# Kernel tuning notes

Measured on AMD Instinct MI355X. Metric: run time of the kernel, lower is better.

Reference implementation:

```python
import jax, jax.numpy as jnp
import numpy as np

FEATURES = 1024
EXPANDED = 16
HIDDEN = FEATURES * EXPANDED  # 16384
BATCH = 4096


def setup_inputs() -> dict:
    key = jax.random.key(0)
    k_x, k_we, k_be, k_wd, k_bd = jax.random.split(key, 5)
    s_enc = 1.0 / np.sqrt(FEATURES)
    s_dec = 1.0 / np.sqrt(HIDDEN)
    return {
        "x": jax.random.normal(k_x, (BATCH, FEATURES), dtype=jnp.float32),
        "W_enc": jax.random.uniform(k_we, (HIDDEN, FEATURES), jnp.float32, -s_enc, s_enc),
        "b_enc": jax.random.uniform(k_be, (HIDDEN,), jnp.float32, -s_enc, s_enc),
        "W_dec": jax.random.uniform(k_wd, (FEATURES, HIDDEN), jnp.float32, -s_dec, s_dec),
        "b_dec": jax.random.uniform(k_bd, (FEATURES,), jnp.float32, -s_dec, s_dec),
        "activate": 64,
    }


def reference(x, W_enc, b_enc, W_dec, b_dec, activate):
    # Encoder: subtract decoder bias, dense GEMM -> pre-activations a [B, HIDDEN]
    xbar = x - b_dec
    a = jnp.einsum("bf,hf->bh", xbar, W_enc) + b_enc
    # TopK per row, relu values, scatter back into a zero tensor
    vals, idx = jax.lax.top_k(a, activate)           # [B, k]
    f = jnp.zeros_like(a)
    rows = jnp.arange(a.shape[0])[:, None]           # [B, 1]
    f = f.at[rows, idx].set(jax.nn.relu(vals))
    # Decoder: dense GEMM back to feature space (faithful to original dense decode)
    xhat = jnp.einsum("bh,fh->bf", f, W_dec) + b_dec
    return f, xhat
```

## Files before the change

kernel.cpp:

```cpp
#include <hip/hip_runtime.h>
#include <cstdint>

#define B_ 4096
#define F_ 1024
#define H_ 16384
#define TOPK 64
#define MAXC 192
#define NBINS 2048
#define BINW 0.00390625f
#define TWOE 0.020f

typedef unsigned short u16;
typedef __attribute__((ext_vector_type(8))) _Float16 f16x8;
typedef __attribute__((ext_vector_type(8))) unsigned short u16x8;
typedef __attribute__((ext_vector_type(4))) float f32x4;

__device__ __forceinline__ u16 f2bf(float f) {
  union { float f; uint32_t u; } v; v.f = f;
  uint32_t u = v.u;
  uint32_t r = u + 0x7FFFu + ((u >> 16) & 1u);
  return (u16)(r >> 16);
}
__device__ __forceinline__ float bf2f(u16 h) {
  union { uint32_t u; float f; } v; v.u = ((uint32_t)h) << 16; return v.f;
}
__device__ __forceinline__ u16 f2h(float f) {
  union { _Float16 h; u16 u; } v; v.h = (_Float16)f; return v.u;
}
__device__ __forceinline__ float h2f(u16 h) {
  union { _Float16 h; u16 u; } v; v.u = h; return (float)v.h;
}

__device__ __forceinline__ void async16(const void* g, void* l) {
  __builtin_amdgcn_global_load_lds(
      reinterpret_cast<const __attribute__((address_space(1))) uint32_t*>(
          reinterpret_cast<uintptr_t>(g)),
      reinterpret_cast<__attribute__((address_space(3))) uint32_t*>(
          reinterpret_cast<uintptr_t>(l)),
      16, 0, 0);
}

__global__ __launch_bounds__(256) void k_xbar(const float* __restrict__ x,
                                              const float* __restrict__ b_dec,
                                              u16* __restrict__ xbar) {
  int i = blockIdx.x * 256 + threadIdx.x;
  int base = i * 4;
  int col = base & (F_ - 1);
  float4 xv = *(const float4*)(x + base);
  float4 bv = *(const float4*)(b_dec + col);
  ushort4 o;
  o.x = f2h(xv.x - bv.x); o.y = f2h(xv.y - bv.y);
  o.z = f2h(xv.z - bv.z); o.w = f2h(xv.w - bv.w);
  *(ushort4*)(xbar + base) = o;
}

__global__ __launch_bounds__(256) void k_cast(const float* __restrict__ src,
                                              u16* __restrict__ dst) {
  size_t base = (size_t)(blockIdx.x * 256 + threadIdx.x) * 4;
  float4 v = *(const float4*)(src + base);
  ushort4 o; o.x = f2h(v.x); o.y = f2h(v.y); o.z = f2h(v.z); o.w = f2h(v.w);
  *(ushort4*)(dst + base) = o;
}

__global__ __launch_bounds__(256) void k_transpose(const float* __restrict__ Wdec,
                                                   u16* __restrict__ WdecT) {
  __shared__ float tile[32][33];
  int hb = blockIdx.x * 32, fb = blockIdx.y * 32;
  int tx = threadIdx.x & 31, ty = threadIdx.x >> 5;
#pragma unroll
  for (int i = 0; i < 32; i += 8)
    tile[ty + i][tx] = Wdec[(size_t)(fb + ty + i) * H_ + hb + tx];
  __syncthreads();
#pragma unroll
  for (int i = 0; i < 32; i += 8)
    WdecT[(size_t)(hb + ty + i) * F_ + fb + tx] = f2bf(tile[tx][ty + i]);
}

__global__ __launch_bounds__(256) void k_gemm(const u16* __restrict__ A,
                                              const u16* __restrict__ Bm,
                                              const float* __restrict__ b_enc,
                                              u16* __restrict__ Cf16,
                                              float* __restrict__ fzero) {
  __shared__ u16 lA[128 * 32];
  __shared__ u16 lB[128 * 32];
  const int tid = threadIdx.x;
  const int lane = tid & 63, wave = tid >> 6;
  const int wm = wave >> 1, wn = wave & 1;
  const int bx = blockIdx.x, by = blockIdx.y;

  const int kcs = (tid & 3) ^ ((tid >> 3) & 3);
  const u16* gA0 = A + (size_t)(by * 128 + (tid >> 2)) * F_ + kcs * 8;
  const u16* gB0 = Bm + (size_t)(bx * 128 + (tid >> 2)) * F_ + kcs * 8;
  u16* lA0 = &lA[tid * 8];
  u16* lB0 = &lB[tid * 8];

  f32x4 acc[4][4] = {};
  const int lm = lane & 15;
  const int kcp = (((lane >> 4) ^ ((lm >> 1) & 3))) * 8;

  for (int k0 = 0; k0 < F_; k0 += 32) {
    async16(gA0 + k0, lA0);
    async16(gA0 + 64 * F_ + k0, lA0 + 2048);
    async16(gB0 + k0, lB0);
    async16(gB0 + 64 * F_ + k0, lB0 + 2048);
    __syncthreads();
    f16x8 av[4], bv[4];
#pragma unroll
    for (int i = 0; i < 4; ++i)
      av[i] = *(const f16x8*)&lA[(wm * 64 + i * 16 + lm) * 32 + kcp];
#pragma unroll
    for (int j = 0; j < 4; ++j)
      bv[j] = *(const f16x8*)&lB[(wn * 64 + j * 16 + lm) * 32 + kcp];
#pragma unroll
    for (int i = 0; i < 4; ++i)
#pragma unroll
      for (int j = 0; j < 4; ++j)
        acc[i][j] = __builtin_amdgcn_mfma_f32_16x16x32_f16(av[i], bv[j], acc[i][j], 0, 0, 0);
    __syncthreads();
  }

  {
    const int bid = by * gridDim.x + bx;
    float* zp = fzero + (size_t)bid * 8192 + tid * 4;
    const f32x4 z4 = {0.f, 0.f, 0.f, 0.f};
#pragma unroll
    for (int k = 0; k < 8; ++k)
      __builtin_nontemporal_store(z4, (f32x4*)(zp + k * 1024));
  }

#pragma unroll
  for (int i = 0; i < 4; ++i) {
    int rowg = by * 128 + wm * 64 + i * 16 + (lane >> 4) * 4;
#pragma unroll
    for (int j = 0; j < 4; ++j) {
      int colg = bx * 128 + wn * 64 + j * 16 + lm;
      float be = b_enc[colg];
      u16* cp = Cf16 + (size_t)rowg * H_ + colg;
#pragma unroll
      for (int r = 0; r < 4; ++r)
        cp[(size_t)r * H_] = f2h(acc[i][j][r] + be);
    }
  }
}

__global__ __launch_bounds__(256) void k_selref(const u16* __restrict__ af16,
                                                const float* __restrict__ x,
                                                const float* __restrict__ b_dec,
                                                const float* __restrict__ Wenc,
                                                const float* __restrict__ b_enc,
                                                int* __restrict__ decIdx,
                                                float* __restrict__ decVal) {
  const int row = blockIdx.x, tid = threadIdx.x;
  const int lane = tid & 63, wave = tid >> 6;
  __shared__ union { u16 sa[H_]; float wbuf[4][2][F_]; } u;
  __shared__ float xs[F_];
  __shared__ int hist[NBINS];
  __shared__ int coarse[256];
  __shared__ double vals[MAXC];
  __shared__ float bes[MAXC];
  __shared__ int idxs[MAXC];
  __shared__ float s_sureCut, s_ambLo;
  __shared__ int s_sure, s_amb;

  for (int i = tid; i < NBINS; i += 256) hist[i] = 0;
  if (tid == 0) { s_sure = 0; s_amb = 0; idxs[0] = 0; }
  for (int k = tid; k < F_; k += 256)
    xs[k] = x[(size_t)row * F_ + k] - b_dec[k];
  __syncthreads();

  const u16* arow = af16 + (size_t)row * H_;
  for (int i = tid; i < H_ / 8; i += 256) {
    u16x8 v = *(const u16x8*)(arow + i * 8);
    *(u16x8*)(u.sa + i * 8) = v;
#pragma unroll
    for (int c = 0; c < 8; ++c) {
      float fv = h2f(v[c]);
      int b = (int)floorf((fv + 4.0f) * 256.0f);
      b = b < 0 ? 0 : (b > NBINS - 1 ? NBINS - 1 : b);
      atomicAdd(&hist[b], 1);
    }
  }
  __syncthreads();
  {
    int s = 0;
#pragma unroll
    for (int j = 0; j < 8; ++j) s += hist[tid * 8 + j];
    coarse[tid] = s;
  }
  __syncthreads();
  if (tid == 0) {
    int c = 0, ifound = 0;
    for (int t = 255; t >= 0; --t) {
      if (c + coarse[t] >= TOPK) {
        for (int b = t * 8 + 7; b >= t * 8; --b) {
          c += hist[b];
          if (c >= TOPK) { ifound = b; break; }
        }
        break;
      }
      c += coarse[t];
    }
    float binlo = (float)ifound * BINW - 4.0f;
    s_sureCut = binlo + BINW + TWOE;
    s_ambLo = binlo - TWOE;
  }
  __syncthreads();

  const float sc = s_sureCut, al = s_ambLo;
  int* dI = decIdx + row * TOPK;
  float* dV = decVal + row * TOPK;
  for (int i = tid; i < H_ / 8; i += 256) {
    u16x8 v = *(const u16x8*)(u.sa + i * 8);
#pragma unroll
    for (int c = 0; c < 8; ++c) {
      float fv = h2f(v[c]);
      if (fv > sc) {
        int p = atomicAdd(&s_sure, 1);
        if (p < TOPK) { dI[p] = i * 8 + c; dV[p] = fv > 0.f ? fv : 0.f; }
      } else if (fv >= al) {
        int p = atomicAdd(&s_amb, 1);
        if (p < MAXC) idxs[p] = i * 8 + c;
      }
    }
  }
  __syncthreads();
  const int S = s_sure < TOPK ? s_sure : TOPK;
  const int cnt = s_amb < MAXC ? s_amb : MAXC;
  for (int c = tid; c < cnt; c += 256) bes[c] = b_enc[idxs[c]];
  __syncthreads();

  float xr[16];
#pragma unroll
  for (int ch = 0; ch < 4; ++ch)
#pragma unroll
    for (int j = 0; j < 4; ++j)
      xr[ch * 4 + j] = xs[ch * 256 + lane * 4 + j];

#define ISSUE_ROW(c_, b_)                                                  \
  {                                                                        \
    int cc_ = (c_) < cnt ? (c_) : 0;                                       \
    const float* src_ = Wenc + (size_t)idxs[cc_] * F_ + lane * 4;          \
    float* dst_ = &u.wbuf[wave][(b_)][lane * 4];                           \
    async16(src_ + 0, dst_ + 0);                                           \
    async16(src_ + 256, dst_ + 256);                                       \
    async16(src_ + 512, dst_ + 512);                                       \
    async16(src_ + 768, dst_ + 768);                                       \
  }

  const int nIter = (cnt - wave + 3) / 4;
  ISSUE_ROW(wave, 0);
  ISSUE_ROW(wave + 4, 1);

  for (int i = 0; i < nIter; ++i) {
    const int c = wave + i * 4;
    const int bsel = i & 1;
    asm volatile("s_waitcnt vmcnt(4)" ::: "memory");
    __builtin_amdgcn_sched_barrier(0);

    const float4* wr = (const float4*)u.wbuf[wave][bsel];
    double s = 0.0;
#pragma unroll
    for (int ch = 0; ch < 4; ++ch) {
      float4 wv = wr[ch * 64 + lane];
      s = fma((double)xr[ch * 4 + 0], (double)wv.x, s);
      s = fma((double)xr[ch * 4 + 1], (double)wv.y, s);
      s = fma((double)xr[ch * 4 + 2], (double)wv.z, s);
      s = fma((double)xr[ch * 4 + 3], (double)wv.w, s);
    }
    __builtin_amdgcn_sched_barrier(0);
    ISSUE_ROW(wave + (i + 2) * 4, bsel);

#pragma unroll
    for (int off = 32; off > 0; off >>= 1) s += __shfl_xor(s, off);
    if (lane == 0 && c < cnt) vals[c] = s + (double)bes[c];
  }
#undef ISSUE_ROW
  __syncthreads();

  const int Kp = TOPK - S;
  for (int c = tid; c < cnt; c += 256) {
    const double v = vals[c];
    const int h = idxs[c];
    int rank = 0;
    for (int o = 0; o < cnt; ++o) {
      double vo = vals[o];
      rank += (vo > v) || (vo == v && idxs[o] < h);
    }
    if (rank < Kp) {
      float fv = v > 0.0 ? (float)v : 0.0f;
      dI[S + rank] = h;
      dV[S + rank] = fv;
    }
  }
}

__global__ __launch_bounds__(256) void k_decode(const int* __restrict__ decIdx,
                                               const float* __restrict__ decVal,
                                               const u16* __restrict__ WdecT,
                                               const float* __restrict__ b_dec,
                                               float* __restrict__ f,
                                               float* __restrict__ xhat) {
  const int row = blockIdx.x, tid = threadIdx.x;
  __shared__ int sIdx[TOPK];
  __shared__ float sVal[TOPK];
  if (tid < TOPK) {
    sIdx[tid] = decIdx[row * TOPK + tid] & (H_ - 1);
    sVal[tid] = decVal[row * TOPK + tid];
  }
  float* frow = f + (size_t)row * H_;
  if (row >= B_ / 2) {
    const f32x4 z4 = {0.f, 0.f, 0.f, 0.f};
    for (int i = tid; i < H_ / 4; i += 256)
      __builtin_nontemporal_store(z4, (f32x4*)frow + i);
  }
  __syncthreads();
  if (tid < TOPK) frow[sIdx[tid]] = sVal[tid];

  const int fb = tid * 4;
  float4 bd = *(const float4*)(b_dec + fb);
  float a0 = bd.x, a1 = bd.y, a2 = bd.z, a3 = bd.w;
#pragma unroll 8
  for (int j = 0; j < TOPK; ++j) {
    const float v = sVal[j];
    const ushort4 w = *(const ushort4*)(WdecT + (size_t)sIdx[j] * F_ + fb);
    a0 += v * bf2f(w.x); a1 += v * bf2f(w.y);
    a2 += v * bf2f(w.z); a3 += v * bf2f(w.w);
  }
  float4 o; o.x = a0; o.y = a1; o.z = a2; o.w = a3;
  *(float4*)(xhat + (size_t)row * F_ + fb) = o;
}

extern "C" void kernel_launch(void* const* d_in, const int* in_sizes, int n_in,
                              void* d_out, int out_size, void* d_ws, size_t ws_size,
                              hipStream_t stream) {
  const float* x    = (const float*)d_in[0];
  const float* Wenc = (const float*)d_in[1];
  const float* benc = (const float*)d_in[2];
  const float* Wdec = (const float*)d_in[3];
  const float* bdec = (const float*)d_in[4];

  float* out  = (float*)d_out;
  float* f    = out;
  float* xhat = out + (size_t)B_ * H_;
  u16* af16 = (u16*)(f + (size_t)B_ * H_ / 2);

  char* ws = (char*)d_ws;
  u16*  xbar    = (u16*)ws;
  u16*  wencb   = (u16*)(ws + (size_t)(8)  * 1048576);
  u16*  wdecT   = (u16*)(ws + (size_t)(40) * 1048576);
  int*  decIdx  = (int*)(ws + (size_t)(76) * 1048576);
  float* decVal = (float*)(ws + (size_t)(77) * 1048576);

  k_xbar<<<B_ * F_ / 1024, 256, 0, stream>>>(x, bdec, xbar);
  k_cast<<<H_ * F_ / 1024, 256, 0, stream>>>(Wenc, wencb);
  k_transpose<<<dim3(H_ / 32, F_ / 32), 256, 0, stream>>>(Wdec, wdecT);
  k_gemm<<<dim3(H_ / 128, B_ / 128), 256, 0, stream>>>(xbar, wencb, benc, af16, f);
  k_selref<<<B_, 256, 0, stream>>>(af16, x, bdec, Wenc, benc, decIdx, decVal);
  k_decode<<<B_, 256, 0, stream>>>(decIdx, decVal, wdecT, bdec, f, xhat);
}
```

Baseline: 761.2 us.

## Triple-buffer encoder GEMM LDS loads and remap workgroups per XCD

Replaces the single-buffered LDS tile loop in the encoder GEMM with a three-stage ring of buffers. Async global-to-LDS copies for later K-steps are issued while MFMAs run on the current one, with a partial vmcnt wait and a single barrier per step. It also switches to a 1D grid whose block index is remapped so that blocks sharing W_enc column tiles land on the same XCD, to improve L2 reuse. This triples LDS use per block, which may lower occupancy, and relies on the K=1024 loop being exactly unrolled into 32 steps.

```diff
diff --git a/kernel.cpp b/kernel.cpp
--- a/kernel.cpp
+++ b/kernel.cpp
@@ -76,52 +76,87 @@
     WdecT[(size_t)(hb + ty + i) * F_ + fb + tx] = f2bf(tile[tx][ty + i]);
 }
 
+__device__ __forceinline__ void gemm_step(const u16* __restrict__ bA,
+                                          const u16* __restrict__ bB,
+                                          int aoff, int boff, int kcp,
+                                          f32x4 (&acc)[4][4]) {
+  f16x8 av[4], bv[4];
+#pragma unroll
+  for (int i = 0; i < 4; ++i)
+    av[i] = *(const f16x8*)&bA[(aoff + i * 16) * 32 + kcp];
+#pragma unroll
+  for (int j = 0; j < 4; ++j)
+    bv[j] = *(const f16x8*)&bB[(boff + j * 16) * 32 + kcp];
+#pragma unroll
+  for (int i = 0; i < 4; ++i)
+#pragma unroll
+    for (int j = 0; j < 4; ++j)
+      acc[i][j] = __builtin_amdgcn_mfma_f32_16x16x32_f16(av[i], bv[j], acc[i][j], 0, 0, 0);
+}
+
 __global__ __launch_bounds__(256) void k_gemm(const u16* __restrict__ A,
                                               const u16* __restrict__ Bm,
                                               const float* __restrict__ b_enc,
                                               u16* __restrict__ Cf16,
                                               float* __restrict__ fzero) {
-  __shared__ u16 lA[128 * 32];
-  __shared__ u16 lB[128 * 32];
+  __shared__ u16 lA[3][128 * 32];
+  __shared__ u16 lB[3][128 * 32];
   const int tid = threadIdx.x;
   const int lane = tid & 63, wave = tid >> 6;
   const int wm = wave >> 1, wn = wave & 1;
-  const int bx = blockIdx.x, by = blockIdx.y;
+  const int wg = blockIdx.x;
+  const int xcd = wg & 7, slot = wg >> 3;
+  const int bx = xcd * 16 + (slot >> 5);
+  const int by = slot & 31;
 
   const int kcs = (tid & 3) ^ ((tid >> 3) & 3);
   const u16* gA0 = A + (size_t)(by * 128 + (tid >> 2)) * F_ + kcs * 8;
   const u16* gB0 = Bm + (size_t)(bx * 128 + (tid >> 2)) * F_ + kcs * 8;
-  u16* lA0 = &lA[tid * 8];
-  u16* lB0 = &lB[tid * 8];
+
+#define STAGE(b_, k0_)                                   \
+  {                                                      \
+    async16(gA0 + (k0_), &lA[b_][tid * 8]);              \
+    async16(gA0 + 64 * F_ + (k0_), &lA[b_][tid * 8 + 2048]); \
+    async16(gB0 + (k0_), &lB[b_][tid * 8]);              \
+    async16(gB0 + 64 * F_ + (k0_), &lB[b_][tid * 8 + 2048]); \
+  }
+#define STEP_SYNC(n_)                                    \
+  {                                                      \
+    asm volatile("s_waitcnt vmcnt(" #n_ ")" ::: "memory"); \
+    __builtin_amdgcn_sched_barrier(0);                   \
+    __builtin_amdgcn_s_barrier();                        \
+    __builtin_amdgcn_sched_barrier(0);                   \
+  }
 
   f32x4 acc[4][4] = {};
   const int lm = lane & 15;
   const int kcp = (((lane >> 4) ^ ((lm >> 1) & 3))) * 8;
-
-  for (int k0 = 0; k0 < F_; k0 += 32) {
-    async16(gA0 + k0, lA0);
-    async16(gA0 + 64 * F_ + k0, lA0 + 2048);
-    async16(gB0 + k0, lB0);
-    async16(gB0 + 64 * F_ + k0, lB0 + 2048);
-    __syncthreads();
-    f16x8 av[4], bv[4];
-#pragma unroll
-    for (int i = 0; i < 4; ++i)
-      av[i] = *(const f16x8*)&lA[(wm * 64 + i * 16 + lm) * 32 + kcp];
-#pragma unroll
-    for (int j = 0; j < 4; ++j)
-      bv[j] = *(const f16x8*)&lB[(wn * 64 + j * 16 + lm) * 32 + kcp];
-#pragma unroll
-    for (int i = 0; i < 4; ++i)
-#pragma unroll
-      for (int j = 0; j < 4; ++j)
-        acc[i][j] = __builtin_amdgcn_mfma_f32_16x16x32_f16(av[i], bv[j], acc[i][j], 0, 0, 0);
-    __syncthreads();
-  }
+  const int aoff = wm * 64 + lm, boff = wn * 64 + lm;
+
+  STAGE(0, 0);
+  STAGE(1, 32);
+  STEP_SYNC(4);
+
+  int kc = 64;
+  for (int s3 = 0; s3 < 30; s3 += 3) {
+    STAGE(2, kc); kc += 32;
+    gemm_step(lA[0], lB[0], aoff, boff, kcp, acc);
+    STEP_SYNC(4);
+    STAGE(0, kc); kc += 32;
+    gemm_step(lA[1], lB[1], aoff, boff, kcp, acc);
+    STEP_SYNC(4);
+    STAGE(1, kc); kc += 32;
+    gemm_step(lA[2], lB[2], aoff, boff, kcp, acc);
+    STEP_SYNC(4);
+  }
+  gemm_step(lA[0], lB[0], aoff, boff, kcp, acc);
+  STEP_SYNC(0);
+  gemm_step(lA[1], lB[1], aoff, boff, kcp, acc);
+#undef STAGE
+#undef STEP_SYNC
 
   {
-    const int bid = by * gridDim.x + bx;
-    float* zp = fzero + (size_t)bid * 8192 + tid * 4;
+    float* zp = fzero + (size_t)wg * 8192 + tid * 4;
     const f32x4 z4 = {0.f, 0.f, 0.f, 0.f};
 #pragma unroll
     for (int k = 0; k < 8; ++k)
@@ -354,7 +389,7 @@
   k_xbar<<<B_ * F_ / 1024, 256, 0, stream>>>(x, bdec, xbar);
   k_cast<<<H_ * F_ / 1024, 256, 0, stream>>>(Wenc, wencb);
   k_transpose<<<dim3(H_ / 32, F_ / 32), 256, 0, stream>>>(Wdec, wdecT);
-  k_gemm<<<dim3(H_ / 128, B_ / 128), 256, 0, stream>>>(xbar, wencb, benc, af16, f);
+  k_gemm<<<4096, 256, 0, stream>>>(xbar, wencb, benc, af16, f);
   k_selref<<<B_, 256, 0, stream>>>(af16, x, bdec, Wenc, benc, decIdx, decVal);
   k_decode<<<B_, 256, 0, stream>>>(decIdx, decVal, wdecT, bdec, f, xhat);
 }
```

New measurement: 806.2 us. +5.9%, slower.

## Replace shared-memory histogram threshold search with register-resident binary search on fp16 keys

Applied to the files above, without the earlier changes.

The per-row top-k threshold was found by building a 2048-bin shared-memory histogram with atomics and then scanning it serially in one thread. Now each thread keeps its 64 fp16 pre-activations in registers as sortable integer keys (negatives clamped to zero) and runs a binary search over the key space, counting elements above the midpoint with wave shuffles and a four-wave reduction. This removes the histogram atomics, the serial scan and the shared-memory staging of the activation row, and it also cuts LDS usage. In exchange it needs about 15 block-wide barrier rounds and adds register pressure. The exact 64th value now sets the sure/ambiguous cutoffs, which can change how many candidates need fp64 refinement.

```diff
diff --git a/kernel.cpp b/kernel.cpp
--- a/kernel.cpp
+++ b/kernel.cpp
@@ -6,8 +6,6 @@
 #define H_ 16384
 #define TOPK 64
 #define MAXC 192
-#define NBINS 2048
-#define BINW 0.00390625f
 #define TWOE 0.020f
 
 typedef unsigned short u16;
@@ -29,6 +27,10 @@
 }
 __device__ __forceinline__ float h2f(u16 h) {
   union { _Float16 h; u16 u; } v; v.u = h; return (float)v.h;
+}
+__device__ __forceinline__ uint32_t key2(uint32_t v) {
+  uint32_t s = (v >> 15) & 0x00010001u;
+  return v & ~(s * 0xFFFFu);
 }
 
 __device__ __forceinline__ void async16(const void* g, void* l) {
@@ -152,74 +154,75 @@
                                                 float* __restrict__ decVal) {
   const int row = blockIdx.x, tid = threadIdx.x;
   const int lane = tid & 63, wave = tid >> 6;
-  __shared__ union { u16 sa[H_]; float wbuf[4][2][F_]; } u;
+  __shared__ float wbuf[4][2][F_];
   __shared__ float xs[F_];
-  __shared__ int hist[NBINS];
-  __shared__ int coarse[256];
   __shared__ double vals[MAXC];
   __shared__ float bes[MAXC];
   __shared__ int idxs[MAXC];
-  __shared__ float s_sureCut, s_ambLo;
+  __shared__ int s_cnt4[4];
   __shared__ int s_sure, s_amb;
 
-  for (int i = tid; i < NBINS; i += 256) hist[i] = 0;
   if (tid == 0) { s_sure = 0; s_amb = 0; idxs[0] = 0; }
   for (int k = tid; k < F_; k += 256)
     xs[k] = x[(size_t)row * F_ + k] - b_dec[k];
-  __syncthreads();
-
-  const u16* arow = af16 + (size_t)row * H_;
-  for (int i = tid; i < H_ / 8; i += 256) {
-    u16x8 v = *(const u16x8*)(arow + i * 8);
-    *(u16x8*)(u.sa + i * 8) = v;
-#pragma unroll
-    for (int c = 0; c < 8; ++c) {
-      float fv = h2f(v[c]);
-      int b = (int)floorf((fv + 4.0f) * 256.0f);
-      b = b < 0 ? 0 : (b > NBINS - 1 ? NBINS - 1 : b);
-      atomicAdd(&hist[b], 1);
-    }
-  }
-  __syncthreads();
+
+  uint32_t pr[32];
   {
-    int s = 0;
-#pragma unroll
-    for (int j = 0; j < 8; ++j) s += hist[tid * 8 + j];
-    coarse[tid] = s;
-  }
-  __syncthreads();
-  if (tid == 0) {
-    int c = 0, ifound = 0;
-    for (int t = 255; t >= 0; --t) {
-      if (c + coarse[t] >= TOPK) {
-        for (int b = t * 8 + 7; b >= t * 8; --b) {
-          c += hist[b];
-          if (c >= TOPK) { ifound = b; break; }
-        }
-        break;
-      }
-      c += coarse[t];
-    }
-    float binlo = (float)ifound * BINW - 4.0f;
-    s_sureCut = binlo + BINW + TWOE;
-    s_ambLo = binlo - TWOE;
-  }
-  __syncthreads();
-
-  const float sc = s_sureCut, al = s_ambLo;
+    const uint4* arow16 = (const uint4*)(af16 + (size_t)row * H_);
+#pragma unroll
+    for (int j = 0; j < 8; ++j) {
+      uint4 v = arow16[tid + 256 * j];
+      pr[j * 4 + 0] = key2(v.x);
+      pr[j * 4 + 1] = key2(v.y);
+      pr[j * 4 + 2] = key2(v.z);
+      pr[j * 4 + 3] = key2(v.w);
+    }
+  }
+
+  uint32_t lo = 0, hi = 0x7C00;
+  while (hi - lo > 1) {
+    const uint32_t mid = (lo + hi) >> 1;
+    int c = 0;
+#pragma unroll
+    for (int r = 0; r < 32; ++r) {
+      c += ((pr[r] & 0xFFFFu) >= mid);
+      c += ((pr[r] >> 16) >= mid);
+    }
+#pragma unroll
+    for (int off = 32; off > 0; off >>= 1) c += __shfl_xor(c, off);
+    if (lane == 0) s_cnt4[wave] = c;
+    __syncthreads();
+    const int tot = s_cnt4[0] + s_cnt4[1] + s_cnt4[2] + s_cnt4[3];
+    if (tot >= TOPK) lo = mid; else hi = mid;
+    __syncthreads();
+  }
+  const float v64f = h2f((u16)lo);
+  const float sc = v64f + TWOE;
+  const float al = v64f - TWOE;
+
   int* dI = decIdx + row * TOPK;
   float* dV = decVal + row * TOPK;
-  for (int i = tid; i < H_ / 8; i += 256) {
-    u16x8 v = *(const u16x8*)(u.sa + i * 8);
-#pragma unroll
-    for (int c = 0; c < 8; ++c) {
-      float fv = h2f(v[c]);
-      if (fv > sc) {
+#pragma unroll
+  for (int j = 0; j < 8; ++j) {
+#pragma unroll
+    for (int w = 0; w < 4; ++w) {
+      const uint32_t v = pr[j * 4 + w];
+      const int ib = (tid + 256 * j) * 8 + w * 2;
+      const float f0 = h2f((u16)(v & 0xFFFFu));
+      const float f1 = h2f((u16)(v >> 16));
+      if (f0 > sc) {
         int p = atomicAdd(&s_sure, 1);
-        if (p < TOPK) { dI[p] = i * 8 + c; dV[p] = fv > 0.f ? fv : 0.f; }
-      } else if (fv >= al) {
+        if (p < TOPK) { dI[p] = ib; dV[p] = f0 > 0.f ? f0 : 0.f; }
+      } else if (f0 >= al) {
         int p = atomicAdd(&s_amb, 1);
-        if (p < MAXC) idxs[p] = i * 8 + c;
+        if (p < MAXC) idxs[p] = ib;
+      }
+      if (f1 > sc) {
+        int p = atomicAdd(&s_sure, 1);
+        if (p < TOPK) { dI[p] = ib + 1; dV[p] = f1 > 0.f ? f1 : 0.f; }
+      } else if (f1 >= al) {
+        int p = atomicAdd(&s_amb, 1);
+        if (p < MAXC) idxs[p] = ib + 1;
       }
     }
   }
@@ -240,7 +243,7 @@
   {                                                                        \
     int cc_ = (c_) < cnt ? (c_) : 0;                                       \
     const float* src_ = Wenc + (size_t)idxs[cc_] * F_ + lane * 4;          \
-    float* dst_ = &u.wbuf[wave][(b_)][lane * 4];                           \
+    float* dst_ = &wbuf[wave][(b_)][lane * 4];                             \
     async16(src_ + 0, dst_ + 0);                                           \
     async16(src_ + 256, dst_ + 256);                                       \
     async16(src_ + 512, dst_ + 512);                                       \
@@ -257,7 +260,7 @@
     asm volatile("s_waitcnt vmcnt(4)" ::: "memory");
     __builtin_amdgcn_sched_barrier(0);
 
-    const float4* wr = (const float4*)u.wbuf[wave][bsel];
+    const float4* wr = (const float4*)wbuf[wave][bsel];
     double s = 0.0;
 #pragma unroll
     for (int ch = 0; ch < 4; ++ch) {
```

Measured after the change: 743.8 us. -2.3%, faster.
